# Performance work log

Hardware: AMD Instinct MI355X
Metric: run time of the kernel (lower is better)

Reference implementation:

```python
import jax, jax.numpy as jnp
import numpy as np

B, M, N, K = 64, 1024, 1024, 128

def setup_inputs() -> dict:
    key = jax.random.key(0)
    k1, k2, k3 = jax.random.split(key, 3)
    # int8 operands (stored as int32 per spec; values fit in int8 range)
    a = jax.random.randint(k1, (B, M, K), 0, 127, dtype=jnp.int32)
    b = jax.random.randint(k2, (B, N, K), 0, 127, dtype=jnp.int32)  # S8N: N-major, matmul uses b^T
    alpha = jax.random.uniform(k3, (1,), dtype=jnp.float32) * 0.01
    return {"a": a, "b": b, "alpha": alpha}

def reference(a, b, alpha):
    acc = jnp.einsum('bmk,bnk->bmn', a, b)  # int32 accumulator
    # fused dequant epilogue: scale by alpha, cast to fp16
    return (alpha[0] * acc.astype(jnp.float32)).astype(jnp.float16)
```

## Files before the change

kernel.cpp:

```cpp
#include <hip/hip_runtime.h>


#define Mdim 1024
#define Ndim 1024
#define Kdim 128
#define NROWS 16
#define NSTRIPS 16
#define BSTRIDE 128
#define WAVEBUF 2048

using int32x4 = __attribute__((ext_vector_type(4))) int;
using floatx4 = __attribute__((ext_vector_type(4))) float;

__device__ __forceinline__ unsigned pack8(int32x4 v) {
    return (unsigned)(v.x & 255) | ((unsigned)(v.y & 255) << 8)
         | ((unsigned)(v.z & 255) << 16) | ((unsigned)(v.w & 255) << 24);
}

__device__ __forceinline__ int swz(int byte_off) {
    return byte_off ^ (((byte_off >> 7) & 7) << 4);
}

__device__ __forceinline__ void wave_lds_fence() {
    asm volatile("s_waitcnt lgkmcnt(0)" ::: "memory");
    __builtin_amdgcn_sched_barrier(0);
}

__global__ __launch_bounds__(512, 2)
void bmm_s8_kernel(const int* __restrict__ A, const int* __restrict__ Bm,
                   const float* __restrict__ alpha_p, float* __restrict__ out)
{
    __shared__ unsigned char Bs[1024 * BSTRIDE];
    __shared__ unsigned char Ws[8 * WAVEBUF];

    const int t    = threadIdx.x;
    const int z    = blockIdx.x;
    const int q    = blockIdx.y;
    const int lane = t & 63;
    const int wave = t >> 6;
    const int wn   = wave * 128;

    const int* __restrict__ Ab = A  + (size_t)z * Mdim * Kdim + (size_t)(q * 256) * Kdim;
    const int* __restrict__ Bb = Bm + (size_t)z * Ndim * Kdim;
    float* __restrict__ Ob     = out + (size_t)z * Mdim * Ndim + (size_t)(q * 256) * Ndim;

    const int r = lane & 15;
    const int g = lane >> 4;

    int32x4 araw[8];
#pragma unroll
    for (int k = 0; k < 8; ++k) {
        const int ks = k >> 2, i = k & 3;
        araw[k] = *(const int32x4*)(Ab + (size_t)r * Kdim + ks * 64 + g * 16 + i * 4);
    }

#pragma unroll 1
    for (int rr = 0; rr < 4; ++rr) {
        int32x4 breg[16];
#pragma unroll
        for (int j = 0; j < 16; ++j) {
            const int f    = lane + 64 * (rr * 16 + j);
            const int row  = wn + (f >> 5);
            const int colb = (f & 31) * 4;
            breg[j] = *(const int32x4*)(Bb + (size_t)row * Kdim + colb);
        }
#pragma unroll
        for (int j = 0; j < 16; ++j) {
            const int f    = lane + 64 * (rr * 16 + j);
            const int row  = wn + (f >> 5);
            const int colb = (f & 31) * 4;
            *(unsigned*)(&Bs[swz(row * BSTRIDE + colb)]) = pack8(breg[j]);
        }
    }
    wave_lds_fence();

    const float alpha = alpha_p[0];
    unsigned char* const Wb = &Ws[wave * WAVEBUF];

#pragma unroll 1
    for (int s = 0; s < NSTRIPS; ++s) {
        int32x4 af[2];
#pragma unroll
        for (int ks = 0; ks < 2; ++ks)
            af[ks] = (int32x4){ (int)pack8(araw[ks * 4 + 0]), (int)pack8(araw[ks * 4 + 1]),
                                (int)pack8(araw[ks * 4 + 2]), (int)pack8(araw[ks * 4 + 3]) };

        if (s + 1 < NSTRIPS) {
            const int* __restrict__ An = Ab + (size_t)((s + 1) * NROWS) * Kdim;
#pragma unroll
            for (int k = 0; k < 8; ++k) {
                const int ks = k >> 2, i = k & 3;
                araw[k] = *(const int32x4*)(An + (size_t)r * Kdim + ks * 64 + g * 16 + i * 4);
            }
        }

        int32x4 acc[8];
#pragma unroll
        for (int nt = 0; nt < 8; ++nt)
            acc[nt] = (int32x4){0, 0, 0, 0};

#pragma unroll
        for (int ks = 0; ks < 2; ++ks) {
#pragma unroll
            for (int nt = 0; nt < 8; ++nt) {
                const int row = wn + nt * 16 + r;
                int32x4 bf = *(const int32x4*)(&Bs[swz(row * BSTRIDE + ks * 64 + g * 16)]);
                acc[nt] = __builtin_amdgcn_mfma_i32_16x16x64_i8(bf, af[ks], acc[nt], 0, 0, 0);
            }
        }

        floatx4 facc[8];
#pragma unroll
        for (int nt = 0; nt < 8; ++nt) {
            facc[nt].x = alpha * (float)acc[nt][0];
            facc[nt].y = alpha * (float)acc[nt][1];
            facc[nt].z = alpha * (float)acc[nt][2];
            facc[nt].w = alpha * (float)acc[nt][3];
        }

#pragma unroll
        for (int c = 0; c < 4; ++c) {
            wave_lds_fence();
            if ((r >> 2) == c) {
                const int rl = r & 3;
#pragma unroll
                for (int nt = 0; nt < 8; ++nt) {
                    const int inrow = nt * 64 + g * 16;
                    *(floatx4*)(&Wb[rl * 512 + (inrow ^ (rl << 4))]) = facc[nt];
                }
            }
            wave_lds_fence();
#pragma unroll
            for (int p = 0; p < 2; ++p) {
                const int rowL  = p * 2 + (lane >> 5);
                const int inrow = (lane & 31) * 16;
                floatx4 v = *(const floatx4*)(&Wb[rowL * 512 + (inrow ^ (rowL << 4))]);
                const size_t fidx = (size_t)(s * NROWS + c * 4 + rowL) * Ndim
                                  + wn + (lane & 31) * 4;
                *(floatx4*)(Ob + fidx) = v;
            }
        }
    }
}

extern "C" void kernel_launch(void* const* d_in, const int* in_sizes, int n_in,
                              void* d_out, int out_size, void* d_ws, size_t ws_size,
                              hipStream_t stream) {
    const int*   a     = (const int*)d_in[0];
    const int*   b     = (const int*)d_in[1];
    const float* alpha = (const float*)d_in[2];
    float*       out   = (float*)d_out;

    const int batch = in_sizes[0] / (Mdim * Kdim);
    dim3 grid(batch, Mdim / (NROWS * NSTRIPS));
    bmm_s8_kernel<<<grid, 512, 0, stream>>>(a, b, alpha, out);
}
```

Before: 334.6 us.

## Hold B fragments in registers and reuse B band LDS for epilogue staging

Each wave now loads its 128-row B band fragments once into registers, so the strip loop no longer reads B from LDS. The band LDS region is then reused as a full 16x128 staging buffer, so the epilogue becomes one write/fence/read pass instead of four quarter passes, cutting fences. Output stores become nontemporal. This adds register pressure (32 extra VGPRs for B fragments) and can reduce occupancy under the 512x2 launch bound.

```diff
diff --git a/kernel.cpp b/kernel.cpp
--- a/kernel.cpp
+++ b/kernel.cpp
@@ -6,8 +6,7 @@
 #define Kdim 128
 #define NROWS 16
 #define NSTRIPS 16
-#define BSTRIDE 128
-#define WAVEBUF 2048
+#define BANDB 16384
 
 using int32x4 = __attribute__((ext_vector_type(4))) int;
 using floatx4 = __attribute__((ext_vector_type(4))) float;
@@ -30,8 +29,7 @@
 void bmm_s8_kernel(const int* __restrict__ A, const int* __restrict__ Bm,
                    const float* __restrict__ alpha_p, float* __restrict__ out)
 {
-    __shared__ unsigned char Bs[1024 * BSTRIDE];
-    __shared__ unsigned char Ws[8 * WAVEBUF];
+    __shared__ unsigned char Bs[8 * BANDB];
 
     const int t    = threadIdx.x;
     const int z    = blockIdx.x;
@@ -47,6 +45,8 @@
     const int r = lane & 15;
     const int g = lane >> 4;
 
+    unsigned char* const band = &Bs[wave * BANDB];
+
     int32x4 araw[8];
 #pragma unroll
     for (int k = 0; k < 8; ++k) {
@@ -60,22 +60,29 @@
 #pragma unroll
         for (int j = 0; j < 16; ++j) {
             const int f    = lane + 64 * (rr * 16 + j);
-            const int row  = wn + (f >> 5);
+            const int row  = f >> 5;
             const int colb = (f & 31) * 4;
-            breg[j] = *(const int32x4*)(Bb + (size_t)row * Kdim + colb);
+            breg[j] = *(const int32x4*)(Bb + (size_t)(wn + row) * Kdim + colb);
         }
 #pragma unroll
         for (int j = 0; j < 16; ++j) {
             const int f    = lane + 64 * (rr * 16 + j);
-            const int row  = wn + (f >> 5);
+            const int row  = f >> 5;
             const int colb = (f & 31) * 4;
-            *(unsigned*)(&Bs[swz(row * BSTRIDE + colb)]) = pack8(breg[j]);
+            *(unsigned*)(&band[swz(row * 128 + colb)]) = pack8(breg[j]);
         }
     }
     wave_lds_fence();
 
+    int32x4 bfrag[8][2];
+#pragma unroll
+    for (int nt = 0; nt < 8; ++nt)
+#pragma unroll
+        for (int ks = 0; ks < 2; ++ks)
+            bfrag[nt][ks] = *(const int32x4*)(
+                &band[(nt * 16 + r) * 128 + (((ks * 4 + g) ^ (r & 7)) << 4)]);
+
     const float alpha = alpha_p[0];
-    unsigned char* const Wb = &Ws[wave * WAVEBUF];
 
 #pragma unroll 1
     for (int s = 0; s < NSTRIPS; ++s) {
@@ -100,14 +107,11 @@
             acc[nt] = (int32x4){0, 0, 0, 0};
 
 #pragma unroll
-        for (int ks = 0; ks < 2; ++ks) {
+        for (int ks = 0; ks < 2; ++ks)
 #pragma unroll
-            for (int nt = 0; nt < 8; ++nt) {
-                const int row = wn + nt * 16 + r;
-                int32x4 bf = *(const int32x4*)(&Bs[swz(row * BSTRIDE + ks * 64 + g * 16)]);
-                acc[nt] = __builtin_amdgcn_mfma_i32_16x16x64_i8(bf, af[ks], acc[nt], 0, 0, 0);
-            }
-        }
+            for (int nt = 0; nt < 8; ++nt)
+                acc[nt] = __builtin_amdgcn_mfma_i32_16x16x64_i8(
+                    bfrag[nt][ks], af[ks], acc[nt], 0, 0, 0);
 
         floatx4 facc[8];
 #pragma unroll
@@ -118,27 +122,18 @@
             facc[nt].w = alpha * (float)acc[nt][3];
         }
 
+        wave_lds_fence();
 #pragma unroll
-        for (int c = 0; c < 4; ++c) {
-            wave_lds_fence();
-            if ((r >> 2) == c) {
-                const int rl = r & 3;
+        for (int nt = 0; nt < 8; ++nt)
+            *(floatx4*)(&band[r * 512 + (((nt * 4 + g) ^ (r & 7)) << 4)]) = facc[nt];
+        wave_lds_fence();
 #pragma unroll
-                for (int nt = 0; nt < 8; ++nt) {
-                    const int inrow = nt * 64 + g * 16;
-                    *(floatx4*)(&Wb[rl * 512 + (inrow ^ (rl << 4))]) = facc[nt];
-                }
-            }
-            wave_lds_fence();
-#pragma unroll
-            for (int p = 0; p < 2; ++p) {
-                const int rowL  = p * 2 + (lane >> 5);
-                const int inrow = (lane & 31) * 16;
-                floatx4 v = *(const floatx4*)(&Wb[rowL * 512 + (inrow ^ (rowL << 4))]);
-                const size_t fidx = (size_t)(s * NROWS + c * 4 + rowL) * Ndim
-                                  + wn + (lane & 31) * 4;
-                *(floatx4*)(Ob + fidx) = v;
-            }
+        for (int p = 0; p < 8; ++p) {
+            const int rw = p * 2 + (lane >> 5);
+            const int u  = lane & 31;
+            floatx4 v = *(const floatx4*)(&band[rw * 512 + ((u ^ (rw & 7)) << 4)]);
+            const size_t fidx = (size_t)(s * NROWS + rw) * Ndim + wn + u * 4;
+            __builtin_nontemporal_store(v, (floatx4*)(Ob + fidx));
         }
     }
 }
```

New measurement: 325.3 us. 2.8% less time.
